# Performance work log

Measured on AMD Instinct MI355X. Metric: run time of the kernel, lower is better.

Reference implementation:

```python
import jax, jax.numpy as jnp
import numpy as np

N, E, H, OUT, L = 50000, 500000, 256, 128, 2
EPS = 1e-5  # torch LayerNorm default


def _make_edges(k):
    # both rows cover all N nodes so that unique()/remap in the original is identity
    k1, k2, kp = jax.random.split(k, 3)
    row0 = jnp.concatenate([jax.random.permutation(kp, N), jax.random.randint(k1, (E - N,), 0, N)])
    row1 = jnp.concatenate([jnp.arange(N), jax.random.randint(k2, (E - N,), 0, N)])
    return jnp.stack([row0, row1]).astype(jnp.int32)


def setup_inputs() -> dict:
    key = jax.random.key(0)
    ks = jax.random.split(key, 7)
    s = 0.02
    x = jax.random.normal(ks[0], (N, H), jnp.float32)
    edge_r1 = _make_edges(ks[1])
    edge_r2 = _make_edges(ks[2])
    Wl = jax.random.normal(ks[3], (L, H, H), jnp.float32) * s
    W0 = jax.random.normal(ks[4], (L, H, H), jnp.float32) * s
    W1 = jax.random.normal(ks[5], (L, H, H), jnp.float32) * s
    bl = jnp.zeros((L, H), jnp.float32)
    b0 = jnp.zeros((L, H), jnp.float32)
    b1 = jnp.zeros((L, H), jnp.float32)
    gamma = jnp.ones((L, H), jnp.float32)
    beta = jnp.zeros((L, H), jnp.float32)
    Wout = jax.random.normal(ks[6], (OUT, H), jnp.float32) * s
    bout = jnp.zeros((OUT,), jnp.float32)
    return dict(x=x, edge_r1=edge_r1, edge_r2=edge_r2, Wl=Wl, bl=bl, W0=W0, b0=b0,
                W1=W1, b1=b1, gamma=gamma, beta=beta, Wout=Wout, bout=bout)


def _layer(i, h, x0, e, Wl, bl, W0, b0, W1, b1, gamma, beta):
    # PyG flow='target_to_source', aggr='add': gather h at e[1], scatter-add at e[0]
    agg = jax.ops.segment_sum(h[e[1]], e[0], num_segments=h.shape[0])  # [N, H]
    z = agg @ Wl[i].T + bl[i] + h @ W0[i].T + b0[i] + x0 @ W1[i].T + b1[i]
    z = jax.nn.relu(z)
    mu = jnp.mean(z, axis=-1, keepdims=True)
    var = jnp.mean(jnp.square(z - mu), axis=-1, keepdims=True)
    return (z - mu) * jax.lax.rsqrt(var + EPS) * gamma[i] + beta[i]  # dropout is identity in eval


def reference(x, edge_r1, edge_r2, Wl, bl, W0, b0, W1, b1, gamma, beta, Wout, bout):
    # reversed(metapath): (C,r2,C) with conv_idx=1 first, then (C,r1,C) with conv_idx=0
    h = _layer(1, x, x, edge_r2, Wl, bl, W0, b0, W1, b1, gamma, beta)
    h = _layer(0, h, x, edge_r1, Wl, bl, W0, b0, W1, b1, gamma, beta)
    return h @ Wout.T + bout  # [N, OUT]
```

## Files before the change

### kernel.cpp

```cpp
#include <hip/hip_runtime.h>
#include <stdint.h>

#define N_NODES 50000
#define N_EDGES 500000
#define NPAD    50048
#define NBLK    128
#define EPB     4096
#define NBUCK   391
#define LFLAT   50048
#define NSC2    196
#define P4CAP   4096
#define EPS     1e-5f

typedef _Float16 half8_ __attribute__((ext_vector_type(8)));
typedef _Float16 half4_ __attribute__((ext_vector_type(4)));
typedef float    float4_ __attribute__((ext_vector_type(4)));

typedef uint32_t u32_g __attribute__((address_space(1)));
typedef uint32_t u32_s __attribute__((address_space(3)));

__device__ __forceinline__ void gload16(const void* g, void* lds_wave_base) {
    __builtin_amdgcn_global_load_lds((const u32_g*)g, (u32_s*)lds_wave_base, 16, 0, 0);
}

__global__ __launch_bounds__(256) void p1_count(const int* __restrict__ e1,
                                                const int* __restrict__ e2,
                                                int* __restrict__ G,
                                                unsigned short* __restrict__ rank16) {
    __shared__ int hist[NBUCK];
    const int bid = blockIdx.x;
    const int s = bid >> 7, blk = bid & 127;
    const int t = threadIdx.x;
    const int* dst = s ? e2 : e1;
    unsigned short* rk = rank16 + (size_t)s * N_EDGES;
    for (int b = t; b < NBUCK; b += 256) hist[b] = 0;
    __syncthreads();
    const int e0 = blk * EPB;
    int myrank[16];
#pragma unroll
    for (int k = 0; k < 16; k++) {
        int i = e0 + k * 256 + t;
        int r = 0;
        if (i < N_EDGES) r = atomicAdd(&hist[dst[i] >> 7], 1);
        myrank[k] = r;
    }
#pragma unroll
    for (int k = 0; k < 16; k++) {
        int i = e0 + k * 256 + t;
        if (i < N_EDGES) rk[i] = (unsigned short)myrank[k];
    }
    __syncthreads();
    int* Gp = G + (s * NBLK + blk) * NBUCK;
    for (int b = t; b < NBUCK; b += 256) Gp[b] = hist[b];
}

__global__ __launch_bounds__(256) void p2_scan(const int* __restrict__ G,
                                               unsigned long long* __restrict__ state,
                                               int* __restrict__ start2) {
    __shared__ int sm[256];
    __shared__ int s_excl;
    const int bid = blockIdx.x;
    const int s = bid / NSC2;
    const int seq = bid % NSC2;
    const int t = threadIdx.x;
    const int i = seq * 256 + t;
    unsigned long long* st = state + s * NSC2;

    int v = 0;
    if (i < LFLAT) v = G[(s * NBLK + (i & 127)) * NBUCK + (i >> 7)];
    sm[t] = v;
    __syncthreads();
    for (int off = 1; off < 256; off <<= 1) {
        int x = sm[t];
        if (t >= off) x += sm[t - off];
        __syncthreads();
        sm[t] = x;
        __syncthreads();
    }
    int total = sm[255];

    if (t == 0) {
        if (seq == 0) {
            atomicExch(&st[0], (2ULL << 32) | (unsigned int)total);
            s_excl = 0;
        } else {
            atomicExch(&st[seq], (1ULL << 32) | (unsigned int)total);
            int running = 0;
            int j = seq - 1;
            while (true) {
                unsigned long long sv = atomicAdd(&st[j], 0ULL);
                unsigned int tag = (unsigned int)(sv >> 32);
                if (tag == 0) continue;
                running += (int)(unsigned int)sv;
                if (tag == 2) break;
                j--;
            }
            atomicExch(&st[seq], (2ULL << 32) | (unsigned int)(running + total));
            s_excl = running;
        }
    }
    __syncthreads();
    if (i < LFLAT) start2[s * LFLAT + i] = s_excl + sm[t] - v;
}

__global__ __launch_bounds__(256) void p3_scatter(const int* __restrict__ e1,
                                                  const int* __restrict__ e2,
                                                  const unsigned short* __restrict__ rank16,
                                                  const int* __restrict__ start2,
                                                  unsigned int* __restrict__ tmp) {
    const int bid = blockIdx.x;
    const int s = bid >> 7, blk = bid & 127;
    const int t = threadIdx.x;
    const int* ed = s ? e2 : e1;
    const int* st = start2 + s * LFLAT;
    const unsigned short* rk = rank16 + (size_t)s * N_EDGES;
    unsigned int* tp = tmp + (size_t)s * N_EDGES;
    const int e0 = blk * EPB;
#pragma unroll
    for (int k = 0; k < 16; k++) {
        int i = e0 + k * 256 + t;
        if (i < N_EDGES) {
            int d   = ed[i];
            int src = ed[N_EDGES + i];
            int pos = st[(d >> 7) * NBLK + blk] + (int)rk[i];
            tp[pos] = ((unsigned)(d & 127) << 16) | (unsigned)src;
        }
    }
}

__global__ __launch_bounds__(256) void p4_build(const unsigned int* __restrict__ tmp,
                                                const int* __restrict__ start2,
                                                int* __restrict__ rp,
                                                int* __restrict__ col) {
    __shared__ int cnt[128];
    __shared__ int off[128];
    __shared__ unsigned int   stM[P4CAP];
    __shared__ unsigned short stS[P4CAP];
    const int b = blockIdx.x;
    const int s = blockIdx.y;
    const int t = threadIdx.x;
    const int* st = start2 + s * LFLAT;
    const int A   = st[b * NBLK];
    const int Bnd = (b == NBUCK - 1) ? N_EDGES : st[(b + 1) * NBLK];
    const unsigned int* tp = tmp + (size_t)s * N_EDGES;

    if (t < 128) cnt[t] = 0;
    __syncthreads();
    for (int eb = A; eb < Bnd; eb += 256) {
        int e = eb + t;
        if (e < Bnd) {
            unsigned v = tp[e];
            int idx = (int)(v >> 16);
            int r = atomicAdd(&cnt[idx], 1);
            int sl = e - A;
            if (sl < P4CAP) {
                stM[sl] = ((unsigned)idx << 12) | (unsigned)r;
                stS[sl] = (unsigned short)(v & 0xFFFFu);
            }
        }
    }
    __syncthreads();
    if (t < 128) off[t] = cnt[t];
    __syncthreads();
    for (int d = 1; d < 128; d <<= 1) {
        int x = 0;
        if (t < 128) { x = off[t]; if (t >= d) x += off[t - d]; }
        __syncthreads();
        if (t < 128) off[t] = x;
        __syncthreads();
    }
    const int nE = Bnd - A;
    int* colS = col + (size_t)s * N_EDGES;
    for (int sl = t; sl < nE && sl < P4CAP; sl += 256) {
        unsigned m = stM[sl];
        int idx = (int)(m >> 12), r = (int)(m & 4095u);
        colS[A + off[idx] - cnt[idx] + r] = (int)stS[sl];
    }
    const int nbase = b * 128;
    if (t < 128 && nbase + t < N_NODES)
        rp[s * (N_NODES + 1) + nbase + t] = A + off[t] - cnt[t];
    if (b == NBUCK - 1 && t == 0) rp[s * (N_NODES + 1) + N_NODES] = N_EDGES;
}

__global__ __launch_bounds__(256) void prep_kernel(
        const float* __restrict__ x, _Float16* __restrict__ xh,
        _Float16* __restrict__ aggb, _Float16* __restrict__ h1,
        const float* __restrict__ Wl, const float* __restrict__ W0,
        const float* __restrict__ W1, const float* __restrict__ Wout,
        _Float16* __restrict__ Wcat,
        const float* __restrict__ bl, const float* __restrict__ b0,
        const float* __restrict__ b1, const float* __restrict__ bout,
        float* __restrict__ bias) {
    const int bid = blockIdx.x;
    const int tid = threadIdx.x;
    if (bid < 12500) {
        int i = bid * 256 + tid;
        float4_ v = ((const float4_*)x)[i];
        half4_ h;
        h[0] = (_Float16)v[0]; h[1] = (_Float16)v[1];
        h[2] = (_Float16)v[2]; h[3] = (_Float16)v[3];
        ((half4_*)xh)[i] = h;
    } else if (bid < 14164) {
        int i = (bid - 12500) * 256 + tid;
        if (i < 2 * 256 * 768) {
            int l = i / (256 * 768);
            int r = i % (256 * 768);
            int j = r / 768, k = r % 768;
            const float* s = (k < 256) ? Wl : (k < 512 ? W0 : W1);
            Wcat[i] = (_Float16)s[l * 65536 + j * 256 + (k & 255)];
        } else {
            Wcat[i] = (_Float16)Wout[i - 2 * 256 * 768];
        }
    } else if (bid < 14200) {
        int j = (bid - 14164) * 256 + tid;
        int buf = j / 3072, jj = j % 3072;
        _Float16* p = (buf == 0) ? xh : (buf == 1) ? aggb : h1;
        half4_ z = {(_Float16)0.f, (_Float16)0.f, (_Float16)0.f, (_Float16)0.f};
        *(half4_*)(p + (size_t)N_NODES * 256 + (size_t)jj * 4) = z;
    } else {
        int i = (bid - 14200) * 256 + tid;
        if (i < 512)      bias[i] = bl[i] + b0[i] + b1[i];
        else if (i < 640) bias[i] = bout[i - 512];
    }
}

__global__ void gather_kernel(const _Float16* __restrict__ hin,
                              const int* __restrict__ rowptr, const int* __restrict__ col,
                              _Float16* __restrict__ dst, int n) {
    int node = blockIdx.x * 4 + (threadIdx.x >> 6);
    int lane = threadIdx.x & 63;
    int half = lane >> 5, l5 = lane & 31;
    if (node >= n) return;
    int s = rowptr[node], e = rowptr[node + 1];
    float a[8] = {0.f, 0.f, 0.f, 0.f, 0.f, 0.f, 0.f, 0.f};
    float b[8] = {0.f, 0.f, 0.f, 0.f, 0.f, 0.f, 0.f, 0.f};
    int i = s + half;
    for (; i + 6 < e; i += 8) {
        int c0 = col[i], c1 = col[i + 2], c2 = col[i + 4], c3 = col[i + 6];
        half8_ v0 = *(const half8_*)(hin + (size_t)c0 * 256 + l5 * 8);
        half8_ v1 = *(const half8_*)(hin + (size_t)c1 * 256 + l5 * 8);
        half8_ v2 = *(const half8_*)(hin + (size_t)c2 * 256 + l5 * 8);
        half8_ v3 = *(const half8_*)(hin + (size_t)c3 * 256 + l5 * 8);
#pragma unroll
        for (int j = 0; j < 8; j++) {
            a[j] += (float)v0[j] + (float)v2[j];
            b[j] += (float)v1[j] + (float)v3[j];
        }
    }
    for (; i < e; i += 2) {
        int c0 = col[i];
        half8_ v0 = *(const half8_*)(hin + (size_t)c0 * 256 + l5 * 8);
#pragma unroll
        for (int j = 0; j < 8; j++) a[j] += (float)v0[j];
    }
    half8_ o;
#pragma unroll
    for (int j = 0; j < 8; j++) {
        float t = a[j] + b[j];
        t += __shfl_xor(t, 32, 64);
        o[j] = (_Float16)t;
    }
    if (half == 0)
        *(half8_*)(dst + (size_t)node * 256 + l5 * 8) = o;
}

__global__ __launch_bounds__(512) void gemm_ln(const _Float16* __restrict__ agg,
                                               const _Float16* __restrict__ hsrc,
                                               const _Float16* __restrict__ xh,
                                               const _Float16* __restrict__ Bw,
                                               const float* __restrict__ bias,
                                               const float* __restrict__ gamma,
                                               const float* __restrict__ beta,
                                               _Float16* __restrict__ H) {
    __shared__ __align__(16) char smem[49152];
    char* AsB = smem;
    char* BsB = smem + 16384;
    const int rowBase = blockIdx.x * 128;
    const int tid  = threadIdx.x;
    const int lane = tid & 63;
    const int w    = tid >> 6;
    const int wm = w & 1, wn = w >> 1;
    const int quad = lane >> 4, mr = lane & 15;
    const int x7 = mr & 7;

    float4_ acc[4][4];
#pragma unroll
    for (int i = 0; i < 4; i++)
#pragma unroll
        for (int j = 0; j < 4; j++) { float4_ z4 = {0.f, 0.f, 0.f, 0.f}; acc[i][j] = z4; }

    int cA0 = w * 64 + lane, cA1 = cA0 + 512;
    int rA0 = cA0 >> 3, rA1 = cA1 >> 3;
    size_t offA0 = (size_t)(rowBase + rA0) * 256 + (((cA0 & 7) ^ (rA0 & 7)) * 8);
    size_t offA1 = (size_t)(rowBase + rA1) * 256 + (((cA1 & 7) ^ (rA1 & 7)) * 8);
    size_t offB[4];
#pragma unroll
    for (int j = 0; j < 4; j++) {
        int c = j * 512 + w * 64 + lane;
        int r = c >> 3;
        offB[j] = (size_t)r * 768 + (((c & 7) ^ (r & 7)) * 8);
    }
    void* lA0 = AsB + w * 1024;
    void* lA1 = AsB + 8192 + w * 1024;

    for (int k0 = 0; k0 < 768; k0 += 64) {
        const _Float16* src = (k0 < 256) ? agg : (k0 < 512) ? hsrc : xh;
        const int kloc = k0 & 255;
        gload16(src + offA0 + kloc, lA0);
        gload16(src + offA1 + kloc, lA1);
        gload16(Bw + offB[0] + k0, BsB + w * 1024);
        gload16(Bw + offB[1] + k0, BsB + 8192 + w * 1024);
        gload16(Bw + offB[2] + k0, BsB + 16384 + w * 1024);
        gload16(Bw + offB[3] + k0, BsB + 24576 + w * 1024);
        __syncthreads();
#pragma unroll
        for (int s = 0; s < 2; s++) {
            half8_ a[4], b[4];
#pragma unroll
            for (int im = 0; im < 4; im++) {
                int row = wm * 64 + im * 16 + mr;
                a[im] = *(const half8_*)(AsB + row * 128 + (((s * 4 + quad) ^ x7) * 16));
            }
#pragma unroll
            for (int in = 0; in < 4; in++) {
                int row = wn * 64 + in * 16 + mr;
                b[in] = *(const half8_*)(BsB + row * 128 + (((s * 4 + quad) ^ x7) * 16));
            }
#pragma unroll
            for (int im = 0; im < 4; im++)
#pragma unroll
                for (int in = 0; in < 4; in++)
                    acc[im][in] = __builtin_amdgcn_mfma_f32_16x16x32_f16(a[im], b[in], acc[im][in], 0, 0, 0);
        }
        __syncthreads();
    }

    float bv[4], gv[4], bev[4];
#pragma unroll
    for (int in = 0; in < 4; in++) {
        int colg = wn * 64 + in * 16 + mr;
        bv[in]  = bias[colg];
        gv[in]  = gamma[colg];
        bev[in] = beta[colg];
    }
    float* lnbuf   = (float*)AsB;
    float* lnstats = (float*)(AsB + 4096);

#pragma unroll
    for (int im = 0; im < 4; im++)
#pragma unroll
        for (int r = 0; r < 4; r++) {
            float s = 0.f, sq = 0.f;
#pragma unroll
            for (int in = 0; in < 4; in++) {
                float v = acc[im][in][r] + bv[in];
                v = v > 0.f ? v : 0.f;
                s += v; sq += v * v;
            }
            s  += __shfl_xor(s, 1, 64);  sq += __shfl_xor(sq, 1, 64);
            s  += __shfl_xor(s, 2, 64);  sq += __shfl_xor(sq, 2, 64);
            s  += __shfl_xor(s, 4, 64);  sq += __shfl_xor(sq, 4, 64);
            s  += __shfl_xor(s, 8, 64);  sq += __shfl_xor(sq, 8, 64);
            if (mr == 0) {
                int rl = wm * 64 + im * 16 + quad * 4 + r;
                lnbuf[(wn * 128 + rl) * 2]     = s;
                lnbuf[(wn * 128 + rl) * 2 + 1] = sq;
            }
        }
    __syncthreads();
    if (tid < 128) {
        float s  = lnbuf[tid * 2]             + lnbuf[(128 + tid) * 2]
                 + lnbuf[(256 + tid) * 2]     + lnbuf[(384 + tid) * 2];
        float sq = lnbuf[tid * 2 + 1]         + lnbuf[(128 + tid) * 2 + 1]
                 + lnbuf[(256 + tid) * 2 + 1] + lnbuf[(384 + tid) * 2 + 1];
        float mu  = s * (1.0f / 256.0f);
        float var = sq * (1.0f / 256.0f) - mu * mu;
        lnstats[tid * 2]     = mu;
        lnstats[tid * 2 + 1] = rsqrtf(var + EPS);
    }
    __syncthreads();

    _Float16* BsH = (_Float16*)BsB;
#pragma unroll
    for (int p = 0; p < 2; p++) {
        if (wm == p) {
#pragma unroll
            for (int im = 0; im < 4; im++)
#pragma unroll
                for (int r = 0; r < 4; r++) {
                    int rl = im * 16 + quad * 4 + r;
                    float mu = lnstats[(p * 64 + rl) * 2];
                    float rs = lnstats[(p * 64 + rl) * 2 + 1];
#pragma unroll
                    for (int in = 0; in < 4; in++) {
                        float v = acc[im][in][r] + bv[in];
                        v = v > 0.f ? v : 0.f;
                        BsH[rl * 256 + wn * 64 + in * 16 + mr] =
                            (_Float16)((v - mu) * rs * gv[in] + bev[in]);
                    }
                }
        }
        __syncthreads();
#pragma unroll
        for (int i = 0; i < 4; i++) {
            int c = i * 512 + tid;
            int row = c >> 5, ch = c & 31;
            half8_ v = *(const half8_*)(BsB + c * 16);
            *(half8_*)(H + (size_t)(rowBase + p * 64 + row) * 256 + ch * 8) = v;
        }
        __syncthreads();
    }
}

__global__ __launch_bounds__(256) void gemm_bt(const _Float16* __restrict__ A, int lda,
                                               const _Float16* __restrict__ B, int ldb,
                                               const float* __restrict__ bias,
                                               float* __restrict__ C, int ldc,
                                               int K, int Mstore) {
    __shared__ _Float16 As[128 * 32];
    __shared__ _Float16 Bs[128 * 32];
    const int rowBase = blockIdx.x * 128;
    const int colBase = blockIdx.y * 128;
    const int tid  = threadIdx.x;
    const int lane = tid & 63;
    const int w    = tid >> 6;
    const int wm = w & 1, wn = w >> 1;
    const int quad = lane >> 4, mr = lane & 15;

    float4_ acc[4][4];
#pragma unroll
    for (int i = 0; i < 4; i++)
#pragma unroll
        for (int j = 0; j < 4; j++) { float4_ z4 = {0.f, 0.f, 0.f, 0.f}; acc[i][j] = z4; }

    const int c0  = w * 64 + lane;
    const int rA0 = c0 >> 2;
    const int ko  = (c0 & 3) * 8;
    char* AsB = (char*)As;
    char* BsB = (char*)Bs;
    void* lA0 = AsB + w * 1024;
    void* lA1 = AsB + 4096 + w * 1024;
    void* lB0 = BsB + w * 1024;
    void* lB1 = BsB + 4096 + w * 1024;
    const _Float16* gA0 = A + (size_t)(rowBase + rA0) * lda + ko;
    const _Float16* gA1 = gA0 + (size_t)64 * lda;
    const _Float16* gB0 = B + (size_t)(colBase + rA0) * ldb + ko;
    const _Float16* gB1 = gB0 + (size_t)64 * ldb;

    for (int k0 = 0; k0 < K; k0 += 32) {
        gload16(gA0 + k0, lA0);
        gload16(gA1 + k0, lA1);
        gload16(gB0 + k0, lB0);
        gload16(gB1 + k0, lB1);
        __syncthreads();
        half8_ a[4], b[4];
#pragma unroll
        for (int im = 0; im < 4; im++)
            a[im] = *(const half8_*)(AsB + ((wm * 64 + im * 16 + mr) * 64 + quad * 16));
#pragma unroll
        for (int in = 0; in < 4; in++)
            b[in] = *(const half8_*)(BsB + ((wn * 64 + in * 16 + mr) * 64 + quad * 16));
#pragma unroll
        for (int im = 0; im < 4; im++)
#pragma unroll
            for (int in = 0; in < 4; in++)
                acc[im][in] = __builtin_amdgcn_mfma_f32_16x16x32_f16(a[im], b[in], acc[im][in], 0, 0, 0);
        __syncthreads();
    }

#pragma unroll
    for (int in = 0; in < 4; in++) {
        const int colg = colBase + wn * 64 + in * 16 + mr;
        const float bv = bias[colg];
#pragma unroll
        for (int im = 0; im < 4; im++) {
            float4_ c = acc[im][in];
#pragma unroll
            for (int r = 0; r < 4; r++) {
                int row = rowBase + wm * 64 + im * 16 + quad * 4 + r;
                if (row < Mstore) C[(size_t)row * ldc + colg] = c[r] + bv;
            }
        }
    }
}

extern "C" void kernel_launch(void* const* d_in, const int* in_sizes, int n_in,
                              void* d_out, int out_size, void* d_ws, size_t ws_size,
                              hipStream_t stream) {
    const float* x    = (const float*)d_in[0];
    const int*   e1   = (const int*)d_in[1];
    const int*   e2   = (const int*)d_in[2];
    const float* Wl   = (const float*)d_in[3];
    const float* bl   = (const float*)d_in[4];
    const float* W0   = (const float*)d_in[5];
    const float* b0   = (const float*)d_in[6];
    const float* W1   = (const float*)d_in[7];
    const float* b1   = (const float*)d_in[8];
    const float* gamma= (const float*)d_in[9];
    const float* beta = (const float*)d_in[10];
    const float* Wout = (const float*)d_in[11];
    const float* bout = (const float*)d_in[12];

    char* ws = (char*)d_ws;
    size_t off = 0;
    auto alloc = [&](size_t bytes) -> char* {
        char* p = ws + off;
        off = (off + bytes + 255) & ~(size_t)255;
        return p;
    };
    _Float16* xh   = (_Float16*)alloc((size_t)NPAD * 256 * 2);
    _Float16* aggb = (_Float16*)alloc((size_t)NPAD * 256 * 2);
    _Float16* h1   = (_Float16*)alloc((size_t)NPAD * 256 * 2);
    _Float16* h2   = (_Float16*)alloc((size_t)NPAD * 256 * 2);
    _Float16* Wcat = (_Float16*)alloc((size_t)(2 * 256 * 768 + 128 * 256) * 2);
    float*    bias = (float*)alloc(640 * 4);
    unsigned long long* states = (unsigned long long*)alloc((size_t)2 * NSC2 * 8);
    int* G      = (int*)alloc((size_t)2 * NBLK * NBUCK * 4);
    int* start2 = (int*)alloc((size_t)2 * LFLAT * 4);
    int* rp     = (int*)alloc((size_t)2 * (N_NODES + 1) * 4);
    unsigned short* rank16 = (unsigned short*)alloc((size_t)2 * N_EDGES * 2);
    unsigned int*   tmp    = (unsigned int*)alloc((size_t)2 * N_EDGES * 4);
    int* col    = (int*)alloc((size_t)2 * N_EDGES * 4);

    int* rp1 = rp, *rp2 = rp + (N_NODES + 1);
    int* col1 = col, *col2 = col + N_EDGES;

    hipMemsetAsync(states, 0, (size_t)2 * NSC2 * 8, stream);

    p1_count<<<256, 256, 0, stream>>>(e1, e2, G, rank16);
    prep_kernel<<<14203, 256, 0, stream>>>(x, xh, aggb, h1,
                                           Wl, W0, W1, Wout, Wcat,
                                           bl, b0, b1, bout, bias);
    p2_scan<<<2 * NSC2, 256, 0, stream>>>(G, states, start2);
    p3_scatter<<<256, 256, 0, stream>>>(e1, e2, rank16, start2, tmp);
    p4_build<<<dim3(NBUCK, 2), 256, 0, stream>>>(tmp, start2, rp, col);

    const int nb4 = (N_NODES + 3) / 4;
    const _Float16* WoutH = Wcat + 393216;

    gather_kernel<<<nb4, 256, 0, stream>>>(xh, rp2, col2, aggb, N_NODES);
    gemm_ln<<<391, 512, 0, stream>>>(aggb, xh, xh, Wcat + 196608,
                                     bias + 256, gamma + 256, beta + 256, h1);
    gather_kernel<<<nb4, 256, 0, stream>>>(h1, rp1, col1, aggb, N_NODES);
    gemm_ln<<<391, 512, 0, stream>>>(aggb, h1, xh, Wcat,
                                     bias, gamma, beta, h2);
    gemm_bt<<<dim3(391, 1), 256, 0, stream>>>(h2, 256, WoutH, 256,
                                              bias + 512, (float*)d_out, 128, 256, N_NODES);
}
```

Before: 325.3 us.

## Fuse output projection into second GEMM+LayerNorm and merge count into prep kernel

```diff
diff --git a/kernel.cpp b/kernel.cpp
--- a/kernel.cpp
+++ b/kernel.cpp
@@ -23,35 +23,72 @@
     __builtin_amdgcn_global_load_lds((const u32_g*)g, (u32_s*)lds_wave_base, 16, 0, 0);
 }
 
-__global__ __launch_bounds__(256) void p1_count(const int* __restrict__ e1,
-                                                const int* __restrict__ e2,
-                                                int* __restrict__ G,
-                                                unsigned short* __restrict__ rank16) {
+__global__ __launch_bounds__(256) void prep_kernel(
+        const int* __restrict__ e1, const int* __restrict__ e2,
+        int* __restrict__ G, unsigned short* __restrict__ rank16,
+        const float* __restrict__ x, _Float16* __restrict__ xh,
+        _Float16* __restrict__ aggb, _Float16* __restrict__ h1,
+        const float* __restrict__ Wl, const float* __restrict__ W0,
+        const float* __restrict__ W1, const float* __restrict__ Wout,
+        _Float16* __restrict__ Wcat,
+        const float* __restrict__ bl, const float* __restrict__ b0,
+        const float* __restrict__ b1, const float* __restrict__ bout,
+        float* __restrict__ bias) {
     __shared__ int hist[NBUCK];
     const int bid = blockIdx.x;
-    const int s = bid >> 7, blk = bid & 127;
-    const int t = threadIdx.x;
-    const int* dst = s ? e2 : e1;
-    unsigned short* rk = rank16 + (size_t)s * N_EDGES;
-    for (int b = t; b < NBUCK; b += 256) hist[b] = 0;
-    __syncthreads();
-    const int e0 = blk * EPB;
-    int myrank[16];
-#pragma unroll
-    for (int k = 0; k < 16; k++) {
-        int i = e0 + k * 256 + t;
-        int r = 0;
-        if (i < N_EDGES) r = atomicAdd(&hist[dst[i] >> 7], 1);
-        myrank[k] = r;
-    }
-#pragma unroll
-    for (int k = 0; k < 16; k++) {
-        int i = e0 + k * 256 + t;
-        if (i < N_EDGES) rk[i] = (unsigned short)myrank[k];
-    }
-    __syncthreads();
-    int* Gp = G + (s * NBLK + blk) * NBUCK;
-    for (int b = t; b < NBUCK; b += 256) Gp[b] = hist[b];
+    const int tid = threadIdx.x;
+    if (bid < 256) {
+        const int s = bid >> 7, blk = bid & 127;
+        const int* dst = s ? e2 : e1;
+        unsigned short* rk = rank16 + (size_t)s * N_EDGES;
+        for (int b = tid; b < NBUCK; b += 256) hist[b] = 0;
+        __syncthreads();
+        const int e0 = blk * EPB;
+        int myrank[16];
+#pragma unroll
+        for (int k = 0; k < 16; k++) {
+            int i = e0 + k * 256 + tid;
+            int r = 0;
+            if (i < N_EDGES) r = atomicAdd(&hist[dst[i] >> 7], 1);
+            myrank[k] = r;
+        }
+#pragma unroll
+        for (int k = 0; k < 16; k++) {
+            int i = e0 + k * 256 + tid;
+            if (i < N_EDGES) rk[i] = (unsigned short)myrank[k];
+        }
+        __syncthreads();
+        int* Gp = G + (s * NBLK + blk) * NBUCK;
+        for (int b = tid; b < NBUCK; b += 256) Gp[b] = hist[b];
+    } else if (bid < 12756) {
+        int i = (bid - 256) * 256 + tid;
+        float4_ v = ((const float4_*)x)[i];
+        half4_ h;
+        h[0] = (_Float16)v[0]; h[1] = (_Float16)v[1];
+        h[2] = (_Float16)v[2]; h[3] = (_Float16)v[3];
+        ((half4_*)xh)[i] = h;
+    } else if (bid < 14420) {
+        int i = (bid - 12756) * 256 + tid;
+        if (i < 2 * 256 * 768) {
+            int l = i / (256 * 768);
+            int r = i % (256 * 768);
+            int j = r / 768, k = r % 768;
+            const float* s = (k < 256) ? Wl : (k < 512 ? W0 : W1);
+            Wcat[i] = (_Float16)s[l * 65536 + j * 256 + (k & 255)];
+        } else {
+            Wcat[i] = (_Float16)Wout[i - 2 * 256 * 768];
+        }
+    } else if (bid < 14456) {
+        int j = (bid - 14420) * 256 + tid;
+        int buf = j / 3072, jj = j % 3072;
+        _Float16* p = (buf == 0) ? xh : (buf == 1) ? aggb : h1;
+        half4_ z = {(_Float16)0.f, (_Float16)0.f, (_Float16)0.f, (_Float16)0.f};
+        *(half4_*)(p + (size_t)N_NODES * 256 + (size_t)jj * 4) = z;
+    } else {
+        int i = (bid - 14456) * 256 + tid;
+        if (i < 512)      bias[i] = bl[i] + b0[i] + b1[i];
+        else if (i < 640) bias[i] = bout[i - 512];
+    }
 }
 
 __global__ __launch_bounds__(256) void p2_scan(const int* __restrict__ G,
@@ -180,48 +217,6 @@
     if (t < 128 && nbase + t < N_NODES)
         rp[s * (N_NODES + 1) + nbase + t] = A + off[t] - cnt[t];
     if (b == NBUCK - 1 && t == 0) rp[s * (N_NODES + 1) + N_NODES] = N_EDGES;
-}
-
-__global__ __launch_bounds__(256) void prep_kernel(
-        const float* __restrict__ x, _Float16* __restrict__ xh,
-        _Float16* __restrict__ aggb, _Float16* __restrict__ h1,
-        const float* __restrict__ Wl, const float* __restrict__ W0,
-        const float* __restrict__ W1, const float* __restrict__ Wout,
-        _Float16* __restrict__ Wcat,
-        const float* __restrict__ bl, const float* __restrict__ b0,
-        const float* __restrict__ b1, const float* __restrict__ bout,
-        float* __restrict__ bias) {
-    const int bid = blockIdx.x;
-    const int tid = threadIdx.x;
-    if (bid < 12500) {
-        int i = bid * 256 + tid;
-        float4_ v = ((const float4_*)x)[i];
-        half4_ h;
-        h[0] = (_Float16)v[0]; h[1] = (_Float16)v[1];
-        h[2] = (_Float16)v[2]; h[3] = (_Float16)v[3];
-        ((half4_*)xh)[i] = h;
-    } else if (bid < 14164) {
-        int i = (bid - 12500) * 256 + tid;
-        if (i < 2 * 256 * 768) {
-            int l = i / (256 * 768);
-            int r = i % (256 * 768);
-            int j = r / 768, k = r % 768;
-            const float* s = (k < 256) ? Wl : (k < 512 ? W0 : W1);
-            Wcat[i] = (_Float16)s[l * 65536 + j * 256 + (k & 255)];
-        } else {
-            Wcat[i] = (_Float16)Wout[i - 2 * 256 * 768];
-        }
-    } else if (bid < 14200) {
-        int j = (bid - 14164) * 256 + tid;
-        int buf = j / 3072, jj = j % 3072;
-        _Float16* p = (buf == 0) ? xh : (buf == 1) ? aggb : h1;
-        half4_ z = {(_Float16)0.f, (_Float16)0.f, (_Float16)0.f, (_Float16)0.f};
-        *(half4_*)(p + (size_t)N_NODES * 256 + (size_t)jj * 4) = z;
-    } else {
-        int i = (bid - 14200) * 256 + tid;
-        if (i < 512)      bias[i] = bl[i] + b0[i] + b1[i];
-        else if (i < 640) bias[i] = bout[i - 512];
-    }
 }
 
 __global__ void gather_kernel(const _Float16* __restrict__ hin,
@@ -271,7 +266,10 @@
                                                const float* __restrict__ bias,
                                                const float* __restrict__ gamma,
                                                const float* __restrict__ beta,
-                                               _Float16* __restrict__ H) {
+                                               _Float16* __restrict__ H,
+                                               const _Float16* __restrict__ Wfin,
+                                               const float* __restrict__ bfin,
+                                               float* __restrict__ outp) {
     __shared__ __align__(16) char smem[49152];
     char* AsB = smem;
     char* BsB = smem + 16384;
@@ -282,6 +280,7 @@
     const int wm = w & 1, wn = w >> 1;
     const int quad = lane >> 4, mr = lane & 15;
     const int x7 = mr & 7;
+    const bool fin = (Wfin != nullptr);
 
     float4_ acc[4][4];
 #pragma unroll
@@ -395,91 +394,51 @@
                     for (int in = 0; in < 4; in++) {
                         float v = acc[im][in][r] + bv[in];
                         v = v > 0.f ? v : 0.f;
-                        BsH[rl * 256 + wn * 64 + in * 16 + mr] =
+                        int cc = wn * 64 + in * 16 + mr;
+                        int addr = fin ? (cc ^ ((rl & 7) << 3)) : cc;
+                        BsH[rl * 256 + addr] =
                             (_Float16)((v - mu) * rs * gv[in] + bev[in]);
                     }
                 }
         }
         __syncthreads();
-#pragma unroll
-        for (int i = 0; i < 4; i++) {
-            int c = i * 512 + tid;
-            int row = c >> 5, ch = c & 31;
-            half8_ v = *(const half8_*)(BsB + c * 16);
-            *(half8_*)(H + (size_t)(rowBase + p * 64 + row) * 256 + ch * 8) = v;
-        }
-        __syncthreads();
-    }
-}
-
-__global__ __launch_bounds__(256) void gemm_bt(const _Float16* __restrict__ A, int lda,
-                                               const _Float16* __restrict__ B, int ldb,
-                                               const float* __restrict__ bias,
-                                               float* __restrict__ C, int ldc,
-                                               int K, int Mstore) {
-    __shared__ _Float16 As[128 * 32];
-    __shared__ _Float16 Bs[128 * 32];
-    const int rowBase = blockIdx.x * 128;
-    const int colBase = blockIdx.y * 128;
-    const int tid  = threadIdx.x;
-    const int lane = tid & 63;
-    const int w    = tid >> 6;
-    const int wm = w & 1, wn = w >> 1;
-    const int quad = lane >> 4, mr = lane & 15;
-
-    float4_ acc[4][4];
-#pragma unroll
-    for (int i = 0; i < 4; i++)
-#pragma unroll
-        for (int j = 0; j < 4; j++) { float4_ z4 = {0.f, 0.f, 0.f, 0.f}; acc[i][j] = z4; }
-
-    const int c0  = w * 64 + lane;
-    const int rA0 = c0 >> 2;
-    const int ko  = (c0 & 3) * 8;
-    char* AsB = (char*)As;
-    char* BsB = (char*)Bs;
-    void* lA0 = AsB + w * 1024;
-    void* lA1 = AsB + 4096 + w * 1024;
-    void* lB0 = BsB + w * 1024;
-    void* lB1 = BsB + 4096 + w * 1024;
-    const _Float16* gA0 = A + (size_t)(rowBase + rA0) * lda + ko;
-    const _Float16* gA1 = gA0 + (size_t)64 * lda;
-    const _Float16* gB0 = B + (size_t)(colBase + rA0) * ldb + ko;
-    const _Float16* gB1 = gB0 + (size_t)64 * ldb;
-
-    for (int k0 = 0; k0 < K; k0 += 32) {
-        gload16(gA0 + k0, lA0);
-        gload16(gA1 + k0, lA1);
-        gload16(gB0 + k0, lB0);
-        gload16(gB1 + k0, lB1);
-        __syncthreads();
-        half8_ a[4], b[4];
-#pragma unroll
-        for (int im = 0; im < 4; im++)
-            a[im] = *(const half8_*)(AsB + ((wm * 64 + im * 16 + mr) * 64 + quad * 16));
-#pragma unroll
-        for (int in = 0; in < 4; in++)
-            b[in] = *(const half8_*)(BsB + ((wn * 64 + in * 16 + mr) * 64 + quad * 16));
-#pragma unroll
-        for (int im = 0; im < 4; im++)
-#pragma unroll
-            for (int in = 0; in < 4; in++)
-                acc[im][in] = __builtin_amdgcn_mfma_f32_16x16x32_f16(a[im], b[in], acc[im][in], 0, 0, 0);
-        __syncthreads();
-    }
-
-#pragma unroll
-    for (int in = 0; in < 4; in++) {
-        const int colg = colBase + wn * 64 + in * 16 + mr;
-        const float bv = bias[colg];
-#pragma unroll
-        for (int im = 0; im < 4; im++) {
-            float4_ c = acc[im][in];
-#pragma unroll
-            for (int r = 0; r < 4; r++) {
-                int row = rowBase + wm * 64 + im * 16 + quad * 4 + r;
-                if (row < Mstore) C[(size_t)row * ldc + colg] = c[r] + bv;
-            }
+        if (!fin) {
+#pragma unroll
+            for (int i = 0; i < 4; i++) {
+                int c = i * 512 + tid;
+                int row = c >> 5, ch = c & 31;
+                half8_ v = *(const half8_*)(BsB + c * 16);
+                *(half8_*)(H + (size_t)(rowBase + p * 64 + row) * 256 + ch * 8) = v;
+            }
+            __syncthreads();
+        } else {
+            float4_ oacc[4];
+#pragma unroll
+            for (int j = 0; j < 4; j++) { float4_ z4 = {0.f, 0.f, 0.f, 0.f}; oacc[j] = z4; }
+            const int rt = w & 3;
+            const int cb = (w >> 2) * 4;
+            const int arow = rt * 16 + mr;
+            const int sw = (arow & 7) << 3;
+#pragma unroll
+            for (int k0 = 0; k0 < 256; k0 += 32) {
+                half8_ av = *(const half8_*)(BsH + arow * 256 + ((k0 + quad * 8) ^ sw));
+#pragma unroll
+                for (int j = 0; j < 4; j++) {
+                    half8_ bv8 = *(const half8_*)(Wfin + (size_t)((cb + j) * 16 + mr) * 256 + k0 + quad * 8);
+                    oacc[j] = __builtin_amdgcn_mfma_f32_16x16x32_f16(av, bv8, oacc[j], 0, 0, 0);
+                }
+            }
+#pragma unroll
+            for (int j = 0; j < 4; j++) {
+                int colg = (cb + j) * 16 + mr;
+                float bb = bfin[colg];
+#pragma unroll
+                for (int r = 0; r < 4; r++) {
+                    int row = rowBase + p * 64 + rt * 16 + quad * 4 + r;
+                    if (row < N_NODES) outp[(size_t)row * 128 + colg] = oacc[j][r] + bb;
+                }
+            }
+            __syncthreads();
         }
     }
 }
@@ -511,7 +470,6 @@
     _Float16* xh   = (_Float16*)alloc((size_t)NPAD * 256 * 2);
     _Float16* aggb = (_Float16*)alloc((size_t)NPAD * 256 * 2);
     _Float16* h1   = (_Float16*)alloc((size_t)NPAD * 256 * 2);
-    _Float16* h2   = (_Float16*)alloc((size_t)NPAD * 256 * 2);
     _Float16* Wcat = (_Float16*)alloc((size_t)(2 * 256 * 768 + 128 * 256) * 2);
     float*    bias = (float*)alloc(640 * 4);
     unsigned long long* states = (unsigned long long*)alloc((size_t)2 * NSC2 * 8);
@@ -527,8 +485,7 @@
 
     hipMemsetAsync(states, 0, (size_t)2 * NSC2 * 8, stream);
 
-    p1_count<<<256, 256, 0, stream>>>(e1, e2, G, rank16);
-    prep_kernel<<<14203, 256, 0, stream>>>(x, xh, aggb, h1,
+    prep_kernel<<<14459, 256, 0, stream>>>(e1, e2, G, rank16, x, xh, aggb, h1,
                                            Wl, W0, W1, Wout, Wcat,
                                            bl, b0, b1, bout, bias);
     p2_scan<<<2 * NSC2, 256, 0, stream>>>(G, states, start2);
@@ -540,10 +497,10 @@
 
     gather_kernel<<<nb4, 256, 0, stream>>>(xh, rp2, col2, aggb, N_NODES);
     gemm_ln<<<391, 512, 0, stream>>>(aggb, xh, xh, Wcat + 196608,
-                                     bias + 256, gamma + 256, beta + 256, h1);
+                                     bias + 256, gamma + 256, beta + 256, h1,
+                                     nullptr, nullptr, nullptr);
     gather_kernel<<<nb4, 256, 0, stream>>>(h1, rp1, col1, aggb, N_NODES);
     gemm_ln<<<391, 512, 0, stream>>>(aggb, h1, xh, Wcat,
-                                     bias, gamma, beta, h2);
-    gemm_bt<<<dim3(391, 1), 256, 0, stream>>>(h2, 256, WoutH, 256,
-                                              bias + 512, (float*)d_out, 128, 256, N_NODES);
-}
+                                     bias, gamma, beta, nullptr,
+                                     WoutH, bias + 512, (float*)d_out);
+}
```

Result: slower. 381.8 us (+17.4%).
